# Performance work log

Hardware: AMD Instinct MI355X
Metric: run time of the kernel (lower is better)

Reference implementation:

```python
import jax, jax.numpy as jnp
import numpy as np

B, S, IN, OUT, H, M = 16, 512, 512, 512, 8, 4
HF = OUT // H  # head_feats = 64


def setup_inputs() -> dict:
    key = jax.random.key(0)
    ks = jax.random.split(key, 12)
    std = 0.02
    queries = jax.random.normal(ks[0], (B, S, IN), jnp.float32)
    keys = jax.random.normal(ks[1], (B, S, IN), jnp.float32)
    timespans = jax.random.uniform(ks[2], (B, S), jnp.float32)
    # causal mask tiled over heads*batch, matching [H*B, S, S] score shape
    attention_masks = jnp.broadcast_to(jnp.tril(jnp.ones((S, S), jnp.float32)), (H * B, S, S))
    event_marks = jax.random.uniform(ks[3], (H * B, 1, S, M), jnp.float32)
    Wq = std * jax.random.normal(ks[4], (IN, OUT), jnp.float32)
    Wk = std * jax.random.normal(ks[5], (IN, OUT), jnp.float32)
    Wv = std * jax.random.normal(ks[6], (IN, OUT), jnp.float32)
    Wt = std * jax.random.normal(ks[7], (IN, OUT), jnp.float32)
    Wi = std * jax.random.normal(ks[8], (HF + 1, M * HF), jnp.float32)  # fc_i weight
    bi = jnp.zeros((M * HF,), jnp.float32)                               # fc_i bias
    weight_i = std * jax.random.normal(ks[9], (M, HF), jnp.float32)
    scale_i = jnp.zeros((M,), jnp.float32)
    return {"queries": queries, "keys": keys, "timespans": timespans,
            "attention_masks": attention_masks, "event_marks": event_marks,
            "Wq": Wq, "Wk": Wk, "Wv": Wv, "Wt": Wt, "Wi": Wi, "bi": bi,
            "weight_i": weight_i, "scale_i": scale_i}


def reference(queries, keys, timespans, attention_masks, event_marks,
              Wq, Wk, Wv, Wt, Wi, bi, weight_i, scale_i):
    # torch's cat(chunk(X, H, dim=2), dim=0) == [B,S,H,HF] -> [H,B,S,HF] -> flat h*B+b
    def split_heads(X):
        return X.reshape(B, S, H, HF).transpose(2, 0, 1, 3)  # [H,B,S,HF]

    Q = split_heads(queries @ Wq)
    K = split_heads(keys @ Wk)
    V = split_heads(keys @ Wv)
    T = split_heads(keys @ Wt)

    scores = jnp.einsum('hbqf,hbkf->hbqk', Q, K) / jnp.sqrt(jnp.float32(OUT))
    mask = attention_masks.reshape(H, B, S, S)
    scores = jnp.where(mask == 0.0, jnp.float32(-2 ** 32 + 1), scores)
    attn = jax.nn.softmax(scores, axis=-1)  # [H,B,Sq,Sk]

    E = jnp.einsum('hbqk,hbkf->hbqf', attn, T)  # events fed to intensity net

    # --- Hawkes intensities ---
    ts = jnp.broadcast_to(timespans[None, :, :, None], (H, B, S, 1))
    mu = jax.nn.sigmoid(jnp.concatenate([E, ts], axis=-1) @ Wi + bi)  # [H,B,S,M*HF]
    mu = mu.reshape(H, B, S, M, HF)  # chunk over marks along feature dim
    scale = jnp.exp(scale_i)  # [M]
    lam = jnp.einsum('hbsmf,mf->hbsm', mu, weight_i) / scale
    lam = scale * jnp.log1p(jnp.exp(lam))  # scaled softplus, [H,B,S,M]

    # mark_inty[h,b,q,k] = sum_m lam[h,b,q,m] * event_marks[h,b,k,m]
    em = event_marks.reshape(H, B, S, M)
    mark_inty = jnp.einsum('hbqm,hbkm->hbqk', lam, em)

    out = jnp.einsum('hbqk,hbkf->hbqf', attn * mark_inty, V)
    out = out.transpose(1, 2, 0, 3).reshape(B, S, OUT) + queries[..., :OUT]
    all_mark_inty = lam.reshape(H * B, S, M)
    return out, all_mark_inty
```

## Files before the change

kernel.cpp:

```cpp
#include <hip/hip_runtime.h>
#include <math.h>

typedef __attribute__((ext_vector_type(8))) short short8;
typedef __attribute__((ext_vector_type(4))) float f32x4;

#define L2E 1.4426950408889634f

static __device__ __forceinline__ unsigned short f2bf(float f) {
  unsigned int u = __float_as_uint(f);
  u += 0x7FFFu + ((u >> 16) & 1u);
  return (unsigned short)(u >> 16);
}

static __device__ __forceinline__ float fast_exp2(float x) {
#if __has_builtin(__builtin_amdgcn_exp2f)
  return __builtin_amdgcn_exp2f(x);
#else
  return exp2f(x);
#endif
}
static __device__ __forceinline__ float fast_rcp(float x) {
  return __builtin_amdgcn_rcpf(x);
}

static __device__ __forceinline__ void cp16(void* lds, const void* g) {
  __builtin_amdgcn_global_load_lds((const __attribute__((address_space(1))) void*)g,
                                   (__attribute__((address_space(3))) void*)lds,
                                   16, 0, 0);
}

__global__ __launch_bounds__(256) void convert_k(
    const float* __restrict__ Wq, const float* __restrict__ Wk,
    const float* __restrict__ Wv, const float* __restrict__ Wt,
    const float* __restrict__ Wi,
    unsigned short* __restrict__ Wb, unsigned short* __restrict__ WiF)
{
  __shared__ unsigned short tr[64 * 68];
  const int blk = blockIdx.x, tid = threadIdx.x;
  if (blk < 256) {
    int which = blk >> 6, tile = blk & 63;
    int r0 = (tile >> 3) << 6, c0 = (tile & 7) << 6;
    const float* W = (which == 0) ? Wq : (which == 1) ? Wk : (which == 2) ? Wv : Wt;
    const int rr = tid >> 4, cc = (tid & 15) << 2;
#pragma unroll
    for (int u = 0; u < 4; ++u) {
      int r = rr + u * 16;
      float4 v = *(const float4*)(W + (size_t)(r0 + r) * 512 + c0 + cc);
      tr[(cc + 0) * 68 + r] = f2bf(v.x);
      tr[(cc + 1) * 68 + r] = f2bf(v.y);
      tr[(cc + 2) * 68 + r] = f2bf(v.z);
      tr[(cc + 3) * 68 + r] = f2bf(v.w);
    }
    __syncthreads();
    unsigned short* dst = Wb + which * 262144;
#pragma unroll
    for (int u = 0; u < 4; ++u) {
      int c = rr + u * 16;
      ushort4 o = *(const ushort4*)&tr[c * 68 + cc];
      *(ushort4*)(dst + (size_t)(c0 + c) * 512 + r0 + cc) = o;
    }
  } else {
    int e = (blk - 256) * 256 + tid;
    int j = e & 7, ll = (e >> 3) & 63, r = e >> 9;
    int kk = r % 3, nt = r / 3;
    int col = nt * 16 + (ll & 15);
    int k = kk * 32 + (ll >> 4) * 8 + j;
    float val = (k < 64) ? Wi[k * 256 + col] : ((k == 64) ? Wi[16384 + col] : 0.0f);
    WiF[e] = f2bf(val * L2E);
  }
}

__global__ __launch_bounds__(256) void proj_mfma(
    const float* __restrict__ qin, const float* __restrict__ kin,
    const unsigned short* __restrict__ Wb,
    unsigned short* __restrict__ Qg, unsigned short* __restrict__ Kg,
    unsigned short* __restrict__ Vt, unsigned short* __restrict__ Tt)
{
  const int which = blockIdx.z;
  const float* A = (which == 0) ? qin : kin;
  const unsigned short* W = Wb + which * 262144;
  const int row0 = blockIdx.x * 128;
  const int col0 = blockIdx.y * 128;
  const int tid = threadIdx.x;
  const int wv = tid >> 6, l = tid & 63;
  const int quad = l >> 4, lc = l & 15;
  const int wm = wv >> 1, wn = wv & 1;

  __shared__ unsigned short Asm[2][128 * 32];
  __shared__ unsigned short Bsm[2][128 * 32];

  const int e2 = tid + 256;
  const int br0 = tid >> 2, bg0 = (tid & 3) ^ (br0 & 3);
  const int br1 = e2 >> 2,  bg1 = (e2 & 3) ^ (br1 & 3);
  f32x4 acc[4][4] = {};

  cp16(&Bsm[0][tid * 8], W + (size_t)(col0 + br0) * 512 + bg0 * 8);
  cp16(&Bsm[0][e2 * 8], W + (size_t)(col0 + br1) * 512 + bg1 * 8);
#pragma unroll
  for (int u = 0; u < 4; ++u) {
    int i = tid + u * 256, r = i >> 3, c4 = i & 7;
    float4 v = *(const float4*)(A + (size_t)(row0 + r) * 512 + c4 * 4);
    ushort4 o;
    o.x = f2bf(v.x); o.y = f2bf(v.y); o.z = f2bf(v.z); o.w = f2bf(v.w);
    *(ushort4*)&Asm[0][r * 32 + (((c4 >> 1) ^ (r & 3)) << 3) + ((c4 & 1) << 2)] = o;
  }
  __syncthreads();

  const int xk = lc & 3;
  for (int ks = 0; ks < 16; ++ks) {
    const int cur = ks & 1, nxt = cur ^ 1;
    float4 av[4];
    if (ks < 15) {
      const int k1 = (ks + 1) << 5;
      cp16(&Bsm[nxt][tid * 8], W + (size_t)(col0 + br0) * 512 + k1 + bg0 * 8);
      cp16(&Bsm[nxt][e2 * 8], W + (size_t)(col0 + br1) * 512 + k1 + bg1 * 8);
#pragma unroll
      for (int u = 0; u < 4; ++u) {
        int i = tid + u * 256, r = i >> 3, c4 = i & 7;
        av[u] = *(const float4*)(A + (size_t)(row0 + r) * 512 + k1 + c4 * 4);
      }
    }
    short8 a[4], b[4];
#pragma unroll
    for (int mi = 0; mi < 4; ++mi)
      a[mi] = *(const short8*)&Asm[cur][(wm * 64 + mi * 16 + lc) * 32 + ((quad ^ xk) << 3)];
#pragma unroll
    for (int nj = 0; nj < 4; ++nj)
      b[nj] = *(const short8*)&Bsm[cur][(wn * 64 + nj * 16 + lc) * 32 + ((quad ^ xk) << 3)];
    __builtin_amdgcn_s_setprio(1);
#pragma unroll
    for (int mi = 0; mi < 4; ++mi)
#pragma unroll
      for (int nj = 0; nj < 4; ++nj)
        acc[mi][nj] = __builtin_amdgcn_mfma_f32_16x16x32_bf16(a[mi], b[nj], acc[mi][nj], 0, 0, 0);
    __builtin_amdgcn_s_setprio(0);
    if (ks < 15) {
#pragma unroll
      for (int u = 0; u < 4; ++u) {
        int i = tid + u * 256, r = i >> 3, c4 = i & 7;
        ushort4 o;
        o.x = f2bf(av[u].x); o.y = f2bf(av[u].y); o.z = f2bf(av[u].z); o.w = f2bf(av[u].w);
        *(ushort4*)&Asm[nxt][r * 32 + (((c4 >> 1) ^ (r & 3)) << 3) + ((c4 & 1) << 2)] = o;
      }
    }
    __syncthreads();
  }

  const int h = (col0 >> 6) + wn;
  const int bidx = row0 >> 9;
  const int hb = h * 16 + bidx;
  if (which < 2) {
    unsigned short* C = (which == 0) ? Qg : Kg;
    const float os = (which == 0) ? 0.044194173824159216f * L2E : 1.0f;
#pragma unroll
    for (int mi = 0; mi < 4; ++mi) {
      int sbase = (row0 & 511) + wm * 64 + mi * 16 + quad * 4;
#pragma unroll
      for (int nj = 0; nj < 4; ++nj) {
        size_t base = (size_t)hb * 32768 + (size_t)sbase * 64 + nj * 16 + lc;
#pragma unroll
        for (int reg = 0; reg < 4; ++reg)
          C[base + (size_t)reg * 64] = f2bf(acc[mi][nj][reg] * os);
      }
    }
  } else {
    unsigned short* C = (which == 2) ? Vt : Tt;
    unsigned short* scr = wn ? Bsm[0] : Asm[0];
    const int sb = (row0 & 511) + wm * 64;
    __syncthreads();
#pragma unroll
    for (int round = 0; round < 2; ++round) {
      if (wm == round) {
#pragma unroll
        for (int mi = 0; mi < 4; ++mi)
#pragma unroll
          for (int nj = 0; nj < 4; ++nj)
#pragma unroll
            for (int reg = 0; reg < 4; ++reg) {
              int f = nj * 16 + lc, s = mi * 16 + quad * 4 + reg;
              int g = (s >> 3) ^ (f & 7);
              scr[f * 64 + g * 8 + (s & 7)] = f2bf(acc[mi][nj][reg]);
            }
#pragma unroll
        for (int it = 0; it < 8; ++it) {
          int fl = it * 8 + (l >> 3);
          int gg = (l & 7) ^ (fl & 7);
          short8 v = *(const short8*)&scr[fl * 64 + gg * 8];
          *(short8*)(C + (size_t)hb * 32768 + (size_t)fl * 512 + sb + (l & 7) * 8) = v;
        }
      }
      __syncthreads();
    }
  }
}

__global__ __launch_bounds__(256, 2) void attn_fused(
    const unsigned short* __restrict__ Qg, const unsigned short* __restrict__ Kg,
    const unsigned short* __restrict__ Vtg, const unsigned short* __restrict__ Ttg,
    const unsigned short* __restrict__ WiF,
    const float* __restrict__ bi, const float* __restrict__ wim,
    const float* __restrict__ sci, const float* __restrict__ tsp,
    const float* __restrict__ em, const float* __restrict__ queries,
    float* __restrict__ out, float* __restrict__ lamout)
{
  const int hb = blockIdx.x;
  const int y = blockIdx.y;
  const int qb = (y == 0) ? 3 : (y == 1) ? 2 : (y == 2) ? 0 : 1;
  const int q0 = qb << 7;
  const int kts = 2 * qb + 2;
  const int tid = threadIdx.x, wv = tid >> 6, l = tid & 63;
  const int quad = l >> 4, lc = l & 15;
  const int xg = lc & 7;
  const int wrow0 = q0 + wv * 32;

  __shared__ unsigned short Ks[2][4096];
  __shared__ unsigned short TVs[2][4096];
  __shared__ unsigned short Wl[4][3072];
  __shared__ float emS[2][256];

  const int e1 = tid + 256;
  const int sr0 = tid >> 3, sg0 = (tid & 7) ^ (sr0 & 7);
  const int sr1 = e1 >> 3,  sg1 = (e1 & 7) ^ (sr1 & 7);
  const int sqk0 = sr0 * 64 + sg0 * 8,  sqk1 = sr1 * 64 + sg1 * 8;
  const int stv0 = sr0 * 512 + sg0 * 8, stv1 = sr1 * 512 + sg1 * 8;

  const unsigned short* KgB = Kg + (size_t)hb * 32768;
  const unsigned short* TgB = Ttg + (size_t)hb * 32768;
  const unsigned short* VgB = Vtg + (size_t)hb * 32768;

  cp16(&Ks[0][tid * 8], KgB + sqk0);
  cp16(&Ks[0][e1 * 8], KgB + sqk1);
  cp16(&TVs[0][tid * 8], TgB + stv0);
  cp16(&TVs[0][e1 * 8], TgB + stv1);

  short8 aq[2][2];
  {
    const unsigned short* Qp = Qg + (size_t)hb * 32768;
#pragma unroll
    for (int rt = 0; rt < 2; ++rt)
#pragma unroll
      for (int kk = 0; kk < 2; ++kk)
        aq[rt][kk] = *(const short8*)(Qp + (size_t)(wrow0 + rt * 16 + lc) * 64 + (kk * 4 + quad) * 8);
  }
  __syncthreads();

  f32x4 Eacc[2][4] = {};
  float lsum[2][4] = {};

  for (int kt = 0; kt < kts; ++kt) {
    const int cur = kt & 1, nxt = cur ^ 1;
    const int k0 = kt << 6;
    if (kt + 1 < kts) {
      const int k1 = (kt + 1) << 6;
      cp16(&Ks[nxt][tid * 8], KgB + k1 * 64 + sqk0);
      cp16(&Ks[nxt][e1 * 8], KgB + k1 * 64 + sqk1);
      cp16(&TVs[nxt][tid * 8], TgB + k1 + stv0);
      cp16(&TVs[nxt][e1 * 8], TgB + k1 + stv1);
    }
    if (k0 <= wrow0 + 31) {
      f32x4 sc[2][4] = {};
      __builtin_amdgcn_s_setprio(1);
#pragma unroll
      for (int kk = 0; kk < 2; ++kk)
#pragma unroll
        for (int nj = 0; nj < 4; ++nj) {
          const bool l0 = (k0 + nj * 16) <= (wrow0 + 15);
          const bool l1 = (k0 + nj * 16) <= (wrow0 + 31);
          if (l1) {
            short8 b = *(const short8*)&Ks[cur][(nj * 16 + lc) * 64 + ((kk * 4 + quad) ^ xg) * 8];
            if (l0) sc[0][nj] = __builtin_amdgcn_mfma_f32_16x16x32_bf16(aq[0][kk], b, sc[0][nj], 0, 0, 0);
            sc[1][nj] = __builtin_amdgcn_mfma_f32_16x16x32_bf16(aq[1][kk], b, sc[1][nj], 0, 0, 0);
          }
        }
      __builtin_amdgcn_s_setprio(0);
#pragma unroll
      for (int rt = 0; rt < 2; ++rt) {
        const int gq = wrow0 + rt * 16 + quad * 4;
#pragma unroll
        for (int nj = 0; nj < 4; ++nj) {
          const int col = nj * 16 + lc;
          if ((k0 + nj * 16) <= (wrow0 + rt * 16 + 15)) {
#pragma unroll
            for (int reg = 0; reg < 4; ++reg) {
              float pv = fast_exp2(sc[rt][nj][reg]);
              if (k0 + col > gq + reg) pv = 0.0f;
              lsum[rt][reg] += pv;
              int row = rt * 16 + quad * 4 + reg;
              int gp = (nj * 2 + (lc >> 3)) ^ (row & 7);
              Wl[wv][row * 96 + gp * 8 + (lc & 7)] = f2bf(pv);
            }
          } else {
#pragma unroll
            for (int reg = 0; reg < 4; ++reg) {
              int row = rt * 16 + quad * 4 + reg;
              int gp = (nj * 2 + (lc >> 3)) ^ (row & 7);
              Wl[wv][row * 96 + gp * 8 + (lc & 7)] = 0;
            }
          }
        }
      }
      __builtin_amdgcn_s_setprio(1);
#pragma unroll
      for (int rt = 0; rt < 2; ++rt)
#pragma unroll
        for (int kk = 0; kk < 2; ++kk) {
          short8 a = *(const short8*)&Wl[wv][(rt * 16 + lc) * 96 + ((kk * 4 + quad) ^ xg) * 8];
#pragma unroll
          for (int fj = 0; fj < 4; ++fj) {
            short8 b = *(const short8*)&TVs[cur][(fj * 16 + lc) * 64 + ((kk * 4 + quad) ^ xg) * 8];
            Eacc[rt][fj] = __builtin_amdgcn_mfma_f32_16x16x32_bf16(a, b, Eacc[rt][fj], 0, 0, 0);
          }
        }
      __builtin_amdgcn_s_setprio(0);
    }
    __syncthreads();
  }

  float inv[2][4];
#pragma unroll
  for (int rt = 0; rt < 2; ++rt)
#pragma unroll
    for (int reg = 0; reg < 4; ++reg) {
      float s = lsum[rt][reg];
#pragma unroll
      for (int off = 1; off < 16; off <<= 1) s += __shfl_xor(s, off);
      inv[rt][reg] = fast_rcp(s);
    }

#pragma unroll
  for (int rt = 0; rt < 2; ++rt)
#pragma unroll
    for (int reg = 0; reg < 4; ++reg) {
      int row = rt * 16 + quad * 4 + reg;
      int gq = q0 + wv * 32 + rt * 16 + quad * 4;
      unsigned short* rp = &Wl[wv][row * 96];
#pragma unroll
      for (int fj = 0; fj < 4; ++fj) {
        int gp = (fj * 2 + (lc >> 3)) ^ (row & 7);
        rp[gp * 8 + (lc & 7)] = f2bf(Eacc[rt][fj][reg] * inv[rt][reg]);
      }
      float tsv = (lc == 0) ? tsp[(hb & 15) * 512 + gq + reg] : 0.0f;
      int gt = 8 + ((lc >> 3) ^ (row & 3));
      rp[gt * 8 + (lc & 7)] = f2bf(tsv);
      int gz = 8 + ((2 + (lc >> 3)) ^ (row & 3));
      rp[gz * 8 + (lc & 7)] = 0;
    }

  float lam4[2][4][4];
#pragma unroll
  for (int rt = 0; rt < 2; ++rt) {
    short8 ia[3];
    ia[0] = *(const short8*)&Wl[wv][(rt * 16 + lc) * 96 + ((0 + quad) ^ xg) * 8];
    ia[1] = *(const short8*)&Wl[wv][(rt * 16 + lc) * 96 + ((4 + quad) ^ xg) * 8];
    ia[2] = *(const short8*)&Wl[wv][(rt * 16 + lc) * 96 + (8 + (quad ^ (lc & 3))) * 8];
    float lac[4][4] = {};
#pragma unroll
    for (int nt = 0; nt < 16; ++nt) {
      f32x4 iacc = {};
      __builtin_amdgcn_s_setprio(1);
#pragma unroll
      for (int kk = 0; kk < 3; ++kk) {
        short8 b = *(const short8*)(WiF + ((nt * 3 + kk) * 64 + l) * 8);
        iacc = __builtin_amdgcn_mfma_f32_16x16x32_bf16(ia[kk], b, iacc, 0, 0, 0);
      }
      __builtin_amdgcn_s_setprio(0);
      float bvv = bi[nt * 16 + lc] * L2E;
      float wmv = wim[nt * 16 + lc];
#pragma unroll
      for (int reg = 0; reg < 4; ++reg) {
        float mu = fast_rcp(1.0f + fast_exp2(-(iacc[reg] + bvv)));
        lac[reg][nt >> 2] += mu * wmv;
      }
    }
#pragma unroll
    for (int m = 0; m < 4; ++m) {
      float scv = __expf(sci[m]);
      float rscv = fast_rcp(scv);
#pragma unroll
      for (int reg = 0; reg < 4; ++reg) {
        float s = lac[reg][m];
#pragma unroll
        for (int off = 1; off < 16; off <<= 1) s += __shfl_xor(s, off);
        float z = s * rscv;
        float sp = (z > 20.0f) ? z : log1pf(__expf(z));
        lam4[rt][reg][m] = scv * sp;
      }
    }
    if (lc < 4) {
      int gq = q0 + wv * 32 + rt * 16 + quad * 4;
#pragma unroll
      for (int reg = 0; reg < 4; ++reg) {
        float v = (lc == 0) ? lam4[rt][reg][0] : (lc == 1) ? lam4[rt][reg][1]
                : (lc == 2) ? lam4[rt][reg][2] : lam4[rt][reg][3];
        lamout[((size_t)hb * 512 + gq + reg) * 4 + lc] = v;
      }
    }
#pragma unroll
    for (int reg = 0; reg < 4; ++reg)
#pragma unroll
      for (int m = 0; m < 4; ++m)
        lam4[rt][reg][m] *= inv[rt][reg];
  }

  cp16(&Ks[0][tid * 8], KgB + sqk0);
  cp16(&Ks[0][e1 * 8], KgB + sqk1);
  cp16(&TVs[0][tid * 8], VgB + stv0);
  cp16(&TVs[0][e1 * 8], VgB + stv1);
  emS[0][tid] = em[(size_t)hb * 2048 + tid];
  __syncthreads();

  f32x4 Oacc[2][4] = {};
  for (int kt = 0; kt < kts; ++kt) {
    const int cur = kt & 1, nxt = cur ^ 1;
    const int k0 = kt << 6;
    if (kt + 1 < kts) {
      const int k1 = (kt + 1) << 6;
      cp16(&Ks[nxt][tid * 8], KgB + k1 * 64 + sqk0);
      cp16(&Ks[nxt][e1 * 8], KgB + k1 * 64 + sqk1);
      cp16(&TVs[nxt][tid * 8], VgB + k1 + stv0);
      cp16(&TVs[nxt][e1 * 8], VgB + k1 + stv1);
      emS[nxt][tid] = em[(size_t)hb * 2048 + k1 * 4 + tid];
    }
    if (k0 <= wrow0 + 31) {
      f32x4 sc[2][4] = {};
      __builtin_amdgcn_s_setprio(1);
#pragma unroll
      for (int kk = 0; kk < 2; ++kk)
#pragma unroll
        for (int nj = 0; nj < 4; ++nj) {
          const bool l0 = (k0 + nj * 16) <= (wrow0 + 15);
          const bool l1 = (k0 + nj * 16) <= (wrow0 + 31);
          if (l1) {
            short8 b = *(const short8*)&Ks[cur][(nj * 16 + lc) * 64 + ((kk * 4 + quad) ^ xg) * 8];
            if (l0) sc[0][nj] = __builtin_amdgcn_mfma_f32_16x16x32_bf16(aq[0][kk], b, sc[0][nj], 0, 0, 0);
            sc[1][nj] = __builtin_amdgcn_mfma_f32_16x16x32_bf16(aq[1][kk], b, sc[1][nj], 0, 0, 0);
          }
        }
      __builtin_amdgcn_s_setprio(0);
#pragma unroll
      for (int nj = 0; nj < 4; ++nj) {
        const int col = nj * 16 + lc;
        const bool l1 = (k0 + nj * 16) <= (wrow0 + 31);
        float4 emv;
        if (l1) emv = *(const float4*)&emS[cur][col * 4];
#pragma unroll
        for (int rt = 0; rt < 2; ++rt) {
          const int gq = wrow0 + rt * 16 + quad * 4;
          if ((k0 + nj * 16) <= (wrow0 + rt * 16 + 15)) {
#pragma unroll
            for (int reg = 0; reg < 4; ++reg) {
              float pv = fast_exp2(sc[rt][nj][reg]);
              if (k0 + col > gq + reg) pv = 0.0f;
              float mk = lam4[rt][reg][0] * emv.x + lam4[rt][reg][1] * emv.y +
                         lam4[rt][reg][2] * emv.z + lam4[rt][reg][3] * emv.w;
              int row = rt * 16 + quad * 4 + reg;
              int gp = (nj * 2 + (lc >> 3)) ^ (row & 7);
              Wl[wv][row * 96 + gp * 8 + (lc & 7)] = f2bf(pv * mk);
            }
          } else {
#pragma unroll
            for (int reg = 0; reg < 4; ++reg) {
              int row = rt * 16 + quad * 4 + reg;
              int gp = (nj * 2 + (lc >> 3)) ^ (row & 7);
              Wl[wv][row * 96 + gp * 8 + (lc & 7)] = 0;
            }
          }
        }
      }
      __builtin_amdgcn_s_setprio(1);
#pragma unroll
      for (int rt = 0; rt < 2; ++rt)
#pragma unroll
        for (int kk = 0; kk < 2; ++kk) {
          short8 a = *(const short8*)&Wl[wv][(rt * 16 + lc) * 96 + ((kk * 4 + quad) ^ xg) * 8];
#pragma unroll
          for (int fj = 0; fj < 4; ++fj) {
            short8 b = *(const short8*)&TVs[cur][(fj * 16 + lc) * 64 + ((kk * 4 + quad) ^ xg) * 8];
            Oacc[rt][fj] = __builtin_amdgcn_mfma_f32_16x16x32_bf16(a, b, Oacc[rt][fj], 0, 0, 0);
          }
        }
      __builtin_amdgcn_s_setprio(0);
    }
    __syncthreads();
  }

  const int h = hb >> 4, bidx = hb & 15;
#pragma unroll
  for (int rt = 0; rt < 2; ++rt) {
    const int gq = q0 + wv * 32 + rt * 16 + quad * 4;
#pragma unroll
    for (int reg = 0; reg < 4; ++reg) {
      size_t o = (size_t)bidx * 262144 + (size_t)(gq + reg) * 512 + h * 64 + lc;
#pragma unroll
      for (int fj = 0; fj < 4; ++fj)
        out[o + fj * 16] = Oacc[rt][fj][reg] + queries[o + fj * 16];
    }
  }
}

extern "C" void kernel_launch(void* const* d_in, const int* in_sizes, int n_in,
                              void* d_out, int out_size, void* d_ws, size_t ws_size,
                              hipStream_t stream)
{
  (void)in_sizes; (void)n_in; (void)out_size; (void)ws_size;
  const float* queries = (const float*)d_in[0];
  const float* keys    = (const float*)d_in[1];
  const float* tsp     = (const float*)d_in[2];
  const float* em      = (const float*)d_in[4];
  const float* Wq      = (const float*)d_in[5];
  const float* Wk      = (const float*)d_in[6];
  const float* Wv      = (const float*)d_in[7];
  const float* Wt      = (const float*)d_in[8];
  const float* Wi      = (const float*)d_in[9];
  const float* bi      = (const float*)d_in[10];
  const float* wim     = (const float*)d_in[11];
  const float* sci     = (const float*)d_in[12];
  float* out = (float*)d_out;

  char* w = (char*)d_ws;
  unsigned short* Qg  = (unsigned short*)(w + 0);
  unsigned short* Kg  = (unsigned short*)(w + 8388608);
  unsigned short* Vt  = (unsigned short*)(w + 16777216);
  unsigned short* Tt  = (unsigned short*)(w + 25165824);
  unsigned short* Wb  = (unsigned short*)(w + 33554432);
  unsigned short* WiF = (unsigned short*)(w + 35651584);

  convert_k<<<352, 256, 0, stream>>>(Wq, Wk, Wv, Wt, Wi, Wb, WiF);
  proj_mfma<<<dim3(64, 4, 4), 256, 0, stream>>>(queries, keys, Wb, Qg, Kg, Vt, Tt);
  attn_fused<<<dim3(128, 4), 256, 0, stream>>>(Qg, Kg, Vt, Tt, WiF, bi, wim, sci,
                                               tsp, em, queries, out,
                                               out + 4194304);
}
```

Baseline: 305.1 us.

## Remap grids to XCD-aware 1D indexing and hoist K/V prefetch earlier

Both the projection and attention kernels now use a flat 1D grid whose block index is decoded so that blocks sharing input rows (or the same head-batch) land on the same XCD, which is meant to improve L2 locality on the multi-die GPU. The attention kernel also reorders q-block scheduling, mixing long and short causal blocks differently. The first K/V/em tile loads for the second phase are issued before the softmax-normalisation and intensity epilogue instead of after, so that load latency overlaps that work. This assumes the hardware assigns blocks round-robin across 8 XCDs and relies on the LDS buffers not being touched by the epilogue.

```diff
diff --git a/kernel.cpp b/kernel.cpp
--- a/kernel.cpp
+++ b/kernel.cpp
@@ -76,11 +76,15 @@
     unsigned short* __restrict__ Qg, unsigned short* __restrict__ Kg,
     unsigned short* __restrict__ Vt, unsigned short* __restrict__ Tt)
 {
-  const int which = blockIdx.z;
+  const int g = blockIdx.x;
+  const int xcd = g & 7, slot = g >> 3;
+  const int v = slot & 15;
+  const int col0 = (v & 3) << 7;
+  const int which = v >> 2;
+  const int row0 = (xcd * 8 + (slot >> 4)) << 7;
+
   const float* A = (which == 0) ? qin : kin;
   const unsigned short* W = Wb + which * 262144;
-  const int row0 = blockIdx.x * 128;
-  const int col0 = blockIdx.y * 128;
   const int tid = threadIdx.x;
   const int wv = tid >> 6, l = tid & 63;
   const int quad = l >> 4, lc = l & 15;
@@ -99,9 +103,9 @@
 #pragma unroll
   for (int u = 0; u < 4; ++u) {
     int i = tid + u * 256, r = i >> 3, c4 = i & 7;
-    float4 v = *(const float4*)(A + (size_t)(row0 + r) * 512 + c4 * 4);
+    float4 v4 = *(const float4*)(A + (size_t)(row0 + r) * 512 + c4 * 4);
     ushort4 o;
-    o.x = f2bf(v.x); o.y = f2bf(v.y); o.z = f2bf(v.z); o.w = f2bf(v.w);
+    o.x = f2bf(v4.x); o.y = f2bf(v4.y); o.z = f2bf(v4.z); o.w = f2bf(v4.w);
     *(ushort4*)&Asm[0][r * 32 + (((c4 >> 1) ^ (r & 3)) << 3) + ((c4 & 1) << 2)] = o;
   }
   __syncthreads();
@@ -178,15 +182,15 @@
 #pragma unroll
             for (int reg = 0; reg < 4; ++reg) {
               int f = nj * 16 + lc, s = mi * 16 + quad * 4 + reg;
-              int g = (s >> 3) ^ (f & 7);
-              scr[f * 64 + g * 8 + (s & 7)] = f2bf(acc[mi][nj][reg]);
+              int gg = (s >> 3) ^ (f & 7);
+              scr[f * 64 + gg * 8 + (s & 7)] = f2bf(acc[mi][nj][reg]);
             }
 #pragma unroll
         for (int it = 0; it < 8; ++it) {
           int fl = it * 8 + (l >> 3);
           int gg = (l & 7) ^ (fl & 7);
-          short8 v = *(const short8*)&scr[fl * 64 + gg * 8];
-          *(short8*)(C + (size_t)hb * 32768 + (size_t)fl * 512 + sb + (l & 7) * 8) = v;
+          short8 vv = *(const short8*)&scr[fl * 64 + gg * 8];
+          *(short8*)(C + (size_t)hb * 32768 + (size_t)fl * 512 + sb + (l & 7) * 8) = vv;
         }
       }
       __syncthreads();
@@ -203,9 +207,11 @@
     const float* __restrict__ em, const float* __restrict__ queries,
     float* __restrict__ out, float* __restrict__ lamout)
 {
-  const int hb = blockIdx.x;
-  const int y = blockIdx.y;
-  const int qb = (y == 0) ? 3 : (y == 1) ? 2 : (y == 2) ? 0 : 1;
+  const int g = blockIdx.x;
+  const int xcd = g & 7, slot = g >> 3;
+  const int qv = slot & 3;
+  const int hb = xcd * 16 + (slot >> 2);
+  const int qb = (qv == 0) ? 3 : (qv == 1) ? 0 : (qv == 2) ? 2 : 1;
   const int q0 = qb << 7;
   const int kts = 2 * qb + 2;
   const int tid = threadIdx.x, wv = tid >> 6, l = tid & 63;
@@ -316,6 +322,12 @@
     __syncthreads();
   }
 
+  cp16(&Ks[0][tid * 8], KgB + sqk0);
+  cp16(&Ks[0][e1 * 8], KgB + sqk1);
+  cp16(&TVs[0][tid * 8], VgB + stv0);
+  cp16(&TVs[0][e1 * 8], VgB + stv1);
+  emS[0][tid] = em[(size_t)hb * 2048 + tid];
+
   float inv[2][4];
 #pragma unroll
   for (int rt = 0; rt < 2; ++rt)
@@ -402,11 +414,6 @@
         lam4[rt][reg][m] *= inv[rt][reg];
   }
 
-  cp16(&Ks[0][tid * 8], KgB + sqk0);
-  cp16(&Ks[0][e1 * 8], KgB + sqk1);
-  cp16(&TVs[0][tid * 8], VgB + stv0);
-  cp16(&TVs[0][e1 * 8], VgB + stv1);
-  emS[0][tid] = em[(size_t)hb * 2048 + tid];
   __syncthreads();
 
   f32x4 Oacc[2][4] = {};
@@ -526,8 +533,8 @@
   unsigned short* WiF = (unsigned short*)(w + 35651584);
 
   convert_k<<<352, 256, 0, stream>>>(Wq, Wk, Wv, Wt, Wi, Wb, WiF);
-  proj_mfma<<<dim3(64, 4, 4), 256, 0, stream>>>(queries, keys, Wb, Qg, Kg, Vt, Tt);
-  attn_fused<<<dim3(128, 4), 256, 0, stream>>>(Qg, Kg, Vt, Tt, WiF, bi, wim, sci,
-                                               tsp, em, queries, out,
-                                               out + 4194304);
-}
+  proj_mfma<<<1024, 256, 0, stream>>>(queries, keys, Wb, Qg, Kg, Vt, Tt);
+  attn_fused<<<512, 256, 0, stream>>>(Qg, Kg, Vt, Tt, WiF, bi, wim, sci,
+                                      tsp, em, queries, out,
+                                      out + 4194304);
+}
```

Result: slower. 323.1 us (+5.9%).
